# Optimization experiments

Measured on AMD Instinct MI355X. Metric: run time of the kernel, lower is better.

Reference implementation:

```python
import jax, jax.numpy as jnp
import numpy as np

NUM_HEADS = 8
NEG_LARGE = -1e9  # stands in for -inf under the causal mask; masked entries get exactly 0 entmax weight


def _entmax15(z):
    """Exact 1.5-entmax along the last axis (Peters & Martins 2019 sort-based algorithm)."""
    z = z * 0.5
    zs = -jnp.sort(-z, axis=-1)                      # descending sort
    T = z.shape[-1]
    k = jnp.arange(1, T + 1, dtype=z.dtype)
    mean = jnp.cumsum(zs, axis=-1) / k
    mean_sq = jnp.cumsum(zs * zs, axis=-1) / k
    ss = k * (mean_sq - mean * mean)
    delta = (1.0 - ss) / k
    tau = mean - jnp.sqrt(jnp.maximum(delta, 0.0))
    support = jnp.sum(tau <= zs, axis=-1, keepdims=True)      # support size >= 1
    tau_star = jnp.take_along_axis(tau, support - 1, axis=-1)
    return jnp.square(jnp.maximum(z - tau_star, 0.0))


def setup_inputs() -> dict:
    key = jax.random.key(0)
    ks = jax.random.split(key, 9)
    B, T, D, H = 2, 2048, 512, NUM_HEADS
    dk = D // H
    s = 1.0 / np.sqrt(D)
    so = 1.0 / np.sqrt(dk)
    x = jax.random.normal(ks[0], (B, T, D), jnp.float32)
    Wq = jax.random.uniform(ks[1], (D, D), jnp.float32, -s, s)
    bq = jax.random.uniform(ks[2], (D,), jnp.float32, -s, s)
    Wk = jax.random.uniform(ks[3], (D, D), jnp.float32, -s, s)
    bk = jax.random.uniform(ks[4], (D,), jnp.float32, -s, s)
    Wv = jax.random.uniform(ks[5], (D, D), jnp.float32, -s, s)
    bv = jax.random.uniform(ks[6], (D,), jnp.float32, -s, s)
    Wo = jax.random.uniform(ks[7], (dk, D), jnp.float32, -so, so)
    bo = jax.random.uniform(ks[8], (D,), jnp.float32, -so, so)
    return {"x": x, "Wq": Wq, "bq": bq, "Wk": Wk, "bk": bk, "Wv": Wv, "bv": bv, "Wo": Wo, "bo": bo}


def reference(x, Wq, bq, Wk, bk, Wv, bv, Wo, bo):
    B, T, D = x.shape
    H = NUM_HEADS
    dk = D // H
    Q = (x @ Wq + bq).reshape(B, T, H, dk).transpose(0, 2, 1, 3)   # [B,H,T,dk]
    K = (x @ Wk + bk).reshape(B, T, H, dk).transpose(0, 2, 1, 3)
    V = (x @ Wv + bv).reshape(B, T, H, dk).transpose(0, 2, 1, 3)
    scores = jnp.einsum('bhtd,bhsd->bhts', Q, K) / np.float32(np.sqrt(dk))
    causal = jnp.triu(jnp.ones((T, T), bool), k=1)                 # True above diagonal
    scores = jnp.where(causal[None, None, :, :], jnp.float32(NEG_LARGE), scores)
    weights = _entmax15(scores)                                    # [B,H,T,T]
    weights_avg = weights.mean(axis=1)                             # [B,T,T]
    V_combined = V.mean(axis=1)                                    # [B,T,dk]
    out = jnp.einsum('bts,bsd->btd', weights_avg, V_combined)      # [B,T,dk]
    return out @ Wo + bo, weights_avg
```

## Files before the change

kernel.cpp:

```cpp
#include <hip/hip_runtime.h>
#include <hip/hip_bf16.h>
#include <cstdint>

#define B_ 2
#define T_ 2048
#define D_ 512
#define H_ 8
#define DK_ 64
#define TQ_ 4
#define NT_ (T_ / TQ_)
#define M_ (B_ * T_)

__global__ __launch_bounds__(256) void gemm_bias_kernel(
    const float* __restrict__ A, const float* __restrict__ W,
    const float* __restrict__ bias, float* __restrict__ C,
    int M, int N, int K)
{
  __shared__ float As[16][68];
  __shared__ float Bs[16][68];
  const int bm = blockIdx.y * 64;
  const int bn = blockIdx.x * 64;
  const int tid = threadIdx.x;
  const int tx = tid & 15, ty = tid >> 4;
  float acc[4][4] = {};
  for (int k0 = 0; k0 < K; k0 += 16) {
    {
      const int r = tid >> 2;
      const int c = (tid & 3) << 2;
      const float4 a = *reinterpret_cast<const float4*>(&A[(size_t)(bm + r) * K + k0 + c]);
      As[c + 0][r] = a.x; As[c + 1][r] = a.y; As[c + 2][r] = a.z; As[c + 3][r] = a.w;
    }
    {
      const int r = tid >> 4;
      const int c = (tid & 15) << 2;
      *reinterpret_cast<float4*>(&Bs[r][c]) =
          *reinterpret_cast<const float4*>(&W[(size_t)(k0 + r) * N + bn + c]);
    }
    __syncthreads();
#pragma unroll
    for (int kk = 0; kk < 16; ++kk) {
      float av[4], bv[4];
#pragma unroll
      for (int i = 0; i < 4; ++i) av[i] = As[kk][ty * 4 + i];
#pragma unroll
      for (int j = 0; j < 4; ++j) bv[j] = Bs[kk][tx * 4 + j];
#pragma unroll
      for (int i = 0; i < 4; ++i)
#pragma unroll
        for (int j = 0; j < 4; ++j) acc[i][j] += av[i] * bv[j];
    }
    __syncthreads();
  }
#pragma unroll
  for (int i = 0; i < 4; ++i) {
    const int row = bm + ty * 4 + i;
#pragma unroll
    for (int j = 0; j < 4; ++j) {
      const int col = bn + tx * 4 + j;
      C[(size_t)row * N + col] = acc[i][j] + bias[col];
    }
  }
}

__global__ __launch_bounds__(256) void gemm_bias_kernelT(
    const float* __restrict__ A, const float* __restrict__ W,
    const float* __restrict__ bias, float* __restrict__ Ct,
    int M, int N, int K)
{
  __shared__ float As[16][68];
  __shared__ float Bs[16][68];
  const int bm = blockIdx.y * 64;
  const int bn = blockIdx.x * 64;
  const int tid = threadIdx.x;
  const int tx = tid & 15, ty = tid >> 4;
  float acc[4][4] = {};
  for (int k0 = 0; k0 < K; k0 += 16) {
    {
      const int r = tid >> 2;
      const int c = (tid & 3) << 2;
      const float4 a = *reinterpret_cast<const float4*>(&A[(size_t)(bm + r) * K + k0 + c]);
      As[c + 0][r] = a.x; As[c + 1][r] = a.y; As[c + 2][r] = a.z; As[c + 3][r] = a.w;
    }
    {
      const int r = tid >> 4;
      const int c = (tid & 15) << 2;
      *reinterpret_cast<float4*>(&Bs[r][c]) =
          *reinterpret_cast<const float4*>(&W[(size_t)(k0 + r) * N + bn + c]);
    }
    __syncthreads();
#pragma unroll
    for (int kk = 0; kk < 16; ++kk) {
      float av[4], bv[4];
#pragma unroll
      for (int i = 0; i < 4; ++i) av[i] = As[kk][ty * 4 + i];
#pragma unroll
      for (int j = 0; j < 4; ++j) bv[j] = Bs[kk][tx * 4 + j];
#pragma unroll
      for (int i = 0; i < 4; ++i)
#pragma unroll
        for (int j = 0; j < 4; ++j) acc[i][j] += av[i] * bv[j];
    }
    __syncthreads();
  }
#pragma unroll
  for (int j = 0; j < 4; ++j) {
    const int col = bn + tx * 4 + j;
    const float bb = bias[col];
    const float4 v = make_float4(acc[0][j] + bb, acc[1][j] + bb, acc[2][j] + bb, acc[3][j] + bb);
    *reinterpret_cast<float4*>(&Ct[(size_t)col * M + bm + ty * 4]) = v;
  }
}

__global__ __launch_bounds__(256) void vcombine_kernel(const float* __restrict__ V,
                                                       float* __restrict__ Vc)
{
  const int idx = blockIdx.x * 256 + threadIdx.x;
  if (idx >= M_ * DK_) return;
  const int row = idx >> 6, d = idx & 63;
  float s = 0.f;
#pragma unroll
  for (int h = 0; h < H_; ++h) s += V[(size_t)row * D_ + h * DK_ + d];
  Vc[idx] = s * 0.125f;
}

__global__ __launch_bounds__(256, 4)
__attribute__((amdgpu_waves_per_eu(4, 4)))
void attn_kernel(
    const float* __restrict__ Qg, const float* __restrict__ Kt,
    const float* __restrict__ Vc, float* __restrict__ wavg,
    float* __restrict__ attn_out)
{
  __shared__ float sc[TQ_][T_];
  __shared__ float4 qs4[TQ_][16];
  __shared__ float part[4][TQ_][DK_];

  const int tid = threadIdx.x;
  const int b = blockIdx.x & 1;
  const int tile = (NT_ - 1) - (blockIdx.x >> 1);
  const int t0 = tile * TQ_;
  const int nS = t0 + TQ_;
  const int wave = __builtin_amdgcn_readfirstlane(tid >> 6);
  const int lane = tid & 63;
  const int n = t0 + wave + 1;
  float* const scw = &sc[wave][0];

  float wacc[32];
#pragma unroll
  for (int j = 0; j < 32; ++j) wacc[j] = 0.f;

  for (int h = 0; h < H_; ++h) {
    __syncthreads();
    if (tid < TQ_ * 16) {
      const int r = tid >> 4, d4 = tid & 15;
      qs4[r][d4] = *reinterpret_cast<const float4*>(
          &Qg[(size_t)(b * T_ + t0 + r) * D_ + h * DK_ + d4 * 4]);
    }
    __syncthreads();

    for (int s0 = tid * 4; s0 < nS; s0 += 1024) {
      const float* Ktp = &Kt[(size_t)(h * DK_) * M_ + b * T_ + s0];
      float4 acc0 = {}, acc1 = {}, acc2 = {}, acc3 = {};
#pragma unroll 2
      for (int d4 = 0; d4 < 16; ++d4) {
        const float4 q0 = qs4[0][d4];
        const float4 q1 = qs4[1][d4];
        const float4 q2 = qs4[2][d4];
        const float4 q3 = qs4[3][d4];
        const float4 k0 = *reinterpret_cast<const float4*>(Ktp + (size_t)(d4 * 4 + 0) * M_);
        const float4 k1 = *reinterpret_cast<const float4*>(Ktp + (size_t)(d4 * 4 + 1) * M_);
        const float4 k2 = *reinterpret_cast<const float4*>(Ktp + (size_t)(d4 * 4 + 2) * M_);
        const float4 k3 = *reinterpret_cast<const float4*>(Ktp + (size_t)(d4 * 4 + 3) * M_);
#define FMA4(a, qv, kv) a.x = fmaf(qv, kv.x, a.x); a.y = fmaf(qv, kv.y, a.y); \
                        a.z = fmaf(qv, kv.z, a.z); a.w = fmaf(qv, kv.w, a.w)
        FMA4(acc0, q0.x, k0); FMA4(acc0, q0.y, k1); FMA4(acc0, q0.z, k2); FMA4(acc0, q0.w, k3);
        FMA4(acc1, q1.x, k0); FMA4(acc1, q1.y, k1); FMA4(acc1, q1.z, k2); FMA4(acc1, q1.w, k3);
        FMA4(acc2, q2.x, k0); FMA4(acc2, q2.y, k1); FMA4(acc2, q2.z, k2); FMA4(acc2, q2.w, k3);
        FMA4(acc3, q3.x, k0); FMA4(acc3, q3.y, k1); FMA4(acc3, q3.z, k2); FMA4(acc3, q3.w, k3);
#undef FMA4
      }
      acc0.x *= 0.0625f; acc0.y *= 0.0625f; acc0.z *= 0.0625f; acc0.w *= 0.0625f;
      acc1.x *= 0.0625f; acc1.y *= 0.0625f; acc1.z *= 0.0625f; acc1.w *= 0.0625f;
      acc2.x *= 0.0625f; acc2.y *= 0.0625f; acc2.z *= 0.0625f; acc2.w *= 0.0625f;
      acc3.x *= 0.0625f; acc3.y *= 0.0625f; acc3.z *= 0.0625f; acc3.w *= 0.0625f;
      *reinterpret_cast<float4*>(&sc[0][s0]) = acc0;
      *reinterpret_cast<float4*>(&sc[1][s0]) = acc1;
      *reinterpret_cast<float4*>(&sc[2][s0]) = acc2;
      *reinterpret_cast<float4*>(&sc[3][s0]) = acc3;
    }
    __syncthreads();

    float srow[32];
#pragma unroll
    for (int j = 0; j < 32; ++j) {
      if (j * 64 < n) {
        const int s = lane + j * 64;
        const float v = scw[s];
        srow[j] = (s < n) ? v : -1e30f;
      }
    }
    asm volatile("" ::: "memory");

    float mx = -1e30f;
#pragma unroll
    for (int j = 0; j < 32; ++j)
      if (j * 64 < n) mx = fmaxf(mx, srow[j]);
#pragma unroll
    for (int m = 32; m >= 1; m >>= 1) mx = fmaxf(mx, __shfl_xor(mx, m, 64));

    float tau = mx - 1.0f;
#pragma unroll 1
    for (int it = 0; it < 16; ++it) {
      float s1 = 0.f, s2 = 0.f;
#pragma unroll
      for (int j = 0; j < 32; ++j) {
        if (j * 64 < n) {
          const float u = fmaxf(srow[j] - tau, 0.f);
          s1 += u;
          s2 = fmaf(u, u, s2);
        }
      }
#pragma unroll
      for (int m = 32; m >= 1; m >>= 1) {
        s1 += __shfl_xor(s1, m, 64);
        s2 += __shfl_xor(s2, m, 64);
      }
      if (s2 - 1.0f < 1e-5f) break;
      tau += (s2 - 1.0f) / fmaxf(2.f * s1, 1e-12f);
    }
    tau = fminf(tau, mx - 1e-8f);

#pragma unroll
    for (int j = 0; j < 32; ++j) {
      if (j * 64 < n) {
        const float u = fmaxf(srow[j] - tau, 0.f);
        wacc[j] = fmaf(u, u, wacc[j]);
      }
    }
  }
  __syncthreads();

#pragma unroll
  for (int j = 0; j < 32; ++j) scw[lane + j * 64] = wacc[j];
  __syncthreads();

  for (int i4 = tid; i4 < TQ_ * T_ / 4; i4 += 256) {
    const int r = i4 >> 9;
    const int c4 = i4 & 511;
    float4 w = reinterpret_cast<const float4*>(&sc[r][0])[c4];
    w.x *= 0.125f; w.y *= 0.125f; w.z *= 0.125f; w.w *= 0.125f;
    reinterpret_cast<float4*>(&wavg[(size_t)(b * T_ + t0 + r) * T_])[c4] = w;
  }

  {
    const int sg = wave, dd = lane;
    float acc0 = 0.f, acc1 = 0.f, acc2 = 0.f, acc3 = 0.f;
    for (int s = sg; s < nS; s += 4) {
      const float v = Vc[(size_t)(b * T_ + s) * DK_ + dd];
      acc0 += sc[0][s] * v;
      acc1 += sc[1][s] * v;
      acc2 += sc[2][s] * v;
      acc3 += sc[3][s] * v;
    }
    part[sg][0][dd] = acc0;
    part[sg][1][dd] = acc1;
    part[sg][2][dd] = acc2;
    part[sg][3][dd] = acc3;
  }
  __syncthreads();
  {
    const int r = wave, dd = lane;
    const float o = (part[0][r][dd] + part[1][r][dd] + part[2][r][dd] + part[3][r][dd]) * 0.125f;
    attn_out[(size_t)(b * T_ + t0 + r) * DK_ + dd] = o;
  }
}

extern "C" void kernel_launch(void* const* d_in, const int* in_sizes, int n_in,
                              void* d_out, int out_size, void* d_ws, size_t ws_size,
                              hipStream_t stream)
{
  const float* x  = (const float*)d_in[0];
  const float* Wq = (const float*)d_in[1];
  const float* bq = (const float*)d_in[2];
  const float* Wk = (const float*)d_in[3];
  const float* bk = (const float*)d_in[4];
  const float* Wv = (const float*)d_in[5];
  const float* bv = (const float*)d_in[6];
  const float* Wo = (const float*)d_in[7];
  const float* bo = (const float*)d_in[8];
  float* out = (float*)d_out;
  float* ws  = (float*)d_ws;

  float* Q  = ws;
  float* Kt = Q + (size_t)M_ * D_;
  float* V  = Kt + (size_t)D_ * M_;
  float* Vc = V + (size_t)M_ * D_;
  float* AO = Vc + (size_t)M_ * DK_;

  float* out1 = out;
  float* wavg = out + (size_t)M_ * D_;

  const dim3 gp(D_ / 64, M_ / 64);
  gemm_bias_kernel <<<gp, 256, 0, stream>>>(x, Wq, bq, Q,  M_, D_, D_);
  gemm_bias_kernelT<<<gp, 256, 0, stream>>>(x, Wk, bk, Kt, M_, D_, D_);
  gemm_bias_kernel <<<gp, 256, 0, stream>>>(x, Wv, bv, V,  M_, D_, D_);
  vcombine_kernel<<<(M_ * DK_ + 255) / 256, 256, 0, stream>>>(V, Vc);
  attn_kernel<<<B_ * NT_, 256, 0, stream>>>(Q, Kt, Vc, wavg, AO);
  gemm_bias_kernel<<<gp, 256, 0, stream>>>(AO, Wo, bo, out1, M_, D_, DK_);
}
```

Measured before the change: 405.5 us.

## Double query tile to 8 rows, prefetch next-head Q, add exact-support tau steps

Grows the attention block to 8 query rows with 512 threads, so each K column load feeds twice as many rows. The next head's Q slice is double-buffered and loaded during the entmax phase, which removes one barrier per head. The tau solver now starts with three exact support-based closed-form updates before switching to Newton steps, and the iteration cap drops from 16 to 12, aiming for fewer reduction rounds. The trade-offs are higher register pressure from eight float4 accumulators, half as many blocks, and a stop test that now uses the absolute error.

```diff
diff --git a/kernel.cpp b/kernel.cpp
--- a/kernel.cpp
+++ b/kernel.cpp
@@ -7,8 +7,8 @@
 #define D_ 512
 #define H_ 8
 #define DK_ 64
-#define TQ_ 4
-#define NT_ (T_ / TQ_)
+#define TQ_ 8
+#define NTL_ (T_ / TQ_)
 #define M_ (B_ * T_)
 
 __global__ __launch_bounds__(256) void gemm_bias_kernel(
@@ -123,20 +123,19 @@
   Vc[idx] = s * 0.125f;
 }
 
-__global__ __launch_bounds__(256, 4)
-__attribute__((amdgpu_waves_per_eu(4, 4)))
+__global__ __launch_bounds__(512, 4)
 void attn_kernel(
     const float* __restrict__ Qg, const float* __restrict__ Kt,
     const float* __restrict__ Vc, float* __restrict__ wavg,
     float* __restrict__ attn_out)
 {
   __shared__ float sc[TQ_][T_];
-  __shared__ float4 qs4[TQ_][16];
+  __shared__ float4 qs4[2][TQ_][16];
   __shared__ float part[4][TQ_][DK_];
 
   const int tid = threadIdx.x;
   const int b = blockIdx.x & 1;
-  const int tile = (NT_ - 1) - (blockIdx.x >> 1);
+  const int tile = (NTL_ - 1) - (blockIdx.x >> 1);
   const int t0 = tile * TQ_;
   const int nS = t0 + TQ_;
   const int wave = __builtin_amdgcn_readfirstlane(tid >> 6);
@@ -148,46 +147,52 @@
 #pragma unroll
   for (int j = 0; j < 32; ++j) wacc[j] = 0.f;
 
+  if (tid < TQ_ * 16) {
+    const int r = tid >> 4, d4 = tid & 15;
+    qs4[0][r][d4] = *reinterpret_cast<const float4*>(
+        &Qg[(size_t)(b * T_ + t0 + r) * D_ + 0 * DK_ + d4 * 4]);
+  }
+  __syncthreads();
+
   for (int h = 0; h < H_; ++h) {
-    __syncthreads();
-    if (tid < TQ_ * 16) {
-      const int r = tid >> 4, d4 = tid & 15;
-      qs4[r][d4] = *reinterpret_cast<const float4*>(
-          &Qg[(size_t)(b * T_ + t0 + r) * D_ + h * DK_ + d4 * 4]);
-    }
-    __syncthreads();
-
-    for (int s0 = tid * 4; s0 < nS; s0 += 1024) {
+    const int s0 = tid * 4;
+    if (s0 < nS) {
       const float* Ktp = &Kt[(size_t)(h * DK_) * M_ + b * T_ + s0];
-      float4 acc0 = {}, acc1 = {}, acc2 = {}, acc3 = {};
+      float4 a[TQ_];
+#pragma unroll
+      for (int r = 0; r < TQ_; ++r) a[r] = make_float4(0.f, 0.f, 0.f, 0.f);
 #pragma unroll 2
       for (int d4 = 0; d4 < 16; ++d4) {
-        const float4 q0 = qs4[0][d4];
-        const float4 q1 = qs4[1][d4];
-        const float4 q2 = qs4[2][d4];
-        const float4 q3 = qs4[3][d4];
         const float4 k0 = *reinterpret_cast<const float4*>(Ktp + (size_t)(d4 * 4 + 0) * M_);
         const float4 k1 = *reinterpret_cast<const float4*>(Ktp + (size_t)(d4 * 4 + 1) * M_);
         const float4 k2 = *reinterpret_cast<const float4*>(Ktp + (size_t)(d4 * 4 + 2) * M_);
         const float4 k3 = *reinterpret_cast<const float4*>(Ktp + (size_t)(d4 * 4 + 3) * M_);
-#define FMA4(a, qv, kv) a.x = fmaf(qv, kv.x, a.x); a.y = fmaf(qv, kv.y, a.y); \
-                        a.z = fmaf(qv, kv.z, a.z); a.w = fmaf(qv, kv.w, a.w)
-        FMA4(acc0, q0.x, k0); FMA4(acc0, q0.y, k1); FMA4(acc0, q0.z, k2); FMA4(acc0, q0.w, k3);
-        FMA4(acc1, q1.x, k0); FMA4(acc1, q1.y, k1); FMA4(acc1, q1.z, k2); FMA4(acc1, q1.w, k3);
-        FMA4(acc2, q2.x, k0); FMA4(acc2, q2.y, k1); FMA4(acc2, q2.z, k2); FMA4(acc2, q2.w, k3);
-        FMA4(acc3, q3.x, k0); FMA4(acc3, q3.y, k1); FMA4(acc3, q3.z, k2); FMA4(acc3, q3.w, k3);
-#undef FMA4
-      }
-      acc0.x *= 0.0625f; acc0.y *= 0.0625f; acc0.z *= 0.0625f; acc0.w *= 0.0625f;
-      acc1.x *= 0.0625f; acc1.y *= 0.0625f; acc1.z *= 0.0625f; acc1.w *= 0.0625f;
-      acc2.x *= 0.0625f; acc2.y *= 0.0625f; acc2.z *= 0.0625f; acc2.w *= 0.0625f;
-      acc3.x *= 0.0625f; acc3.y *= 0.0625f; acc3.z *= 0.0625f; acc3.w *= 0.0625f;
-      *reinterpret_cast<float4*>(&sc[0][s0]) = acc0;
-      *reinterpret_cast<float4*>(&sc[1][s0]) = acc1;
-      *reinterpret_cast<float4*>(&sc[2][s0]) = acc2;
-      *reinterpret_cast<float4*>(&sc[3][s0]) = acc3;
-    }
-    __syncthreads();
+#pragma unroll
+        for (int r = 0; r < TQ_; ++r) {
+          const float4 q = qs4[h & 1][r][d4];
+          a[r].x = fmaf(q.x, k0.x, a[r].x); a[r].y = fmaf(q.x, k0.y, a[r].y);
+          a[r].z = fmaf(q.x, k0.z, a[r].z); a[r].w = fmaf(q.x, k0.w, a[r].w);
+          a[r].x = fmaf(q.y, k1.x, a[r].x); a[r].y = fmaf(q.y, k1.y, a[r].y);
+          a[r].z = fmaf(q.y, k1.z, a[r].z); a[r].w = fmaf(q.y, k1.w, a[r].w);
+          a[r].x = fmaf(q.z, k2.x, a[r].x); a[r].y = fmaf(q.z, k2.y, a[r].y);
+          a[r].z = fmaf(q.z, k2.z, a[r].z); a[r].w = fmaf(q.z, k2.w, a[r].w);
+          a[r].x = fmaf(q.w, k3.x, a[r].x); a[r].y = fmaf(q.w, k3.y, a[r].y);
+          a[r].z = fmaf(q.w, k3.z, a[r].z); a[r].w = fmaf(q.w, k3.w, a[r].w);
+        }
+      }
+#pragma unroll
+      for (int r = 0; r < TQ_; ++r) {
+        a[r].x *= 0.0625f; a[r].y *= 0.0625f; a[r].z *= 0.0625f; a[r].w *= 0.0625f;
+        *reinterpret_cast<float4*>(&sc[r][s0]) = a[r];
+      }
+    }
+    __syncthreads();
+
+    if (h + 1 < H_ && tid < TQ_ * 16) {
+      const int r = tid >> 4, d4 = tid & 15;
+      qs4[(h + 1) & 1][r][d4] = *reinterpret_cast<const float4*>(
+          &Qg[(size_t)(b * T_ + t0 + r) * D_ + (h + 1) * DK_ + d4 * 4]);
+    }
 
     float srow[32];
 #pragma unroll
@@ -198,7 +203,6 @@
         srow[j] = (s < n) ? v : -1e30f;
       }
     }
-    asm volatile("" ::: "memory");
 
     float mx = -1e30f;
 #pragma unroll
@@ -209,14 +213,15 @@
 
     float tau = mx - 1.0f;
 #pragma unroll 1
-    for (int it = 0; it < 16; ++it) {
-      float s1 = 0.f, s2 = 0.f;
+    for (int it = 0; it < 12; ++it) {
+      float s1 = 0.f, s2 = 0.f, cn = 0.f;
 #pragma unroll
       for (int j = 0; j < 32; ++j) {
         if (j * 64 < n) {
           const float u = fmaxf(srow[j] - tau, 0.f);
           s1 += u;
           s2 = fmaf(u, u, s2);
+          cn += (u > 0.f) ? 1.f : 0.f;
         }
       }
 #pragma unroll
@@ -224,8 +229,17 @@
         s1 += __shfl_xor(s1, m, 64);
         s2 += __shfl_xor(s2, m, 64);
       }
-      if (s2 - 1.0f < 1e-5f) break;
-      tau += (s2 - 1.0f) / fmaxf(2.f * s1, 1e-12f);
+      if (fabsf(s2 - 1.0f) < 1e-5f) break;
+      if (it < 3) {
+#pragma unroll
+        for (int m = 32; m >= 1; m >>= 1) cn += __shfl_xor(cn, m, 64);
+        const float kf = fmaxf(cn, 1.f);
+        const float mu = tau + s1 / kf;
+        const float ss = s2 - s1 * s1 / kf;
+        tau = mu - sqrtf(fmaxf((1.0f - ss) / kf, 0.f));
+      } else {
+        tau += (s2 - 1.0f) / fmaxf(2.f * s1, 1e-12f);
+      }
     }
     tau = fminf(tau, mx - 1e-8f);
 
@@ -236,14 +250,14 @@
         wacc[j] = fmaf(u, u, wacc[j]);
       }
     }
-  }
-  __syncthreads();
+    __syncthreads();
+  }
 
 #pragma unroll
   for (int j = 0; j < 32; ++j) scw[lane + j * 64] = wacc[j];
   __syncthreads();
 
-  for (int i4 = tid; i4 < TQ_ * T_ / 4; i4 += 256) {
+  for (int i4 = tid; i4 < TQ_ * T_ / 4; i4 += 512) {
     const int r = i4 >> 9;
     const int c4 = i4 & 511;
     float4 w = reinterpret_cast<const float4*>(&sc[r][0])[c4];
@@ -252,25 +266,27 @@
   }
 
   {
-    const int sg = wave, dd = lane;
-    float acc0 = 0.f, acc1 = 0.f, acc2 = 0.f, acc3 = 0.f;
+    const int sg = wave & 3;
+    const int rb = (wave >> 2) * 4;
+    float a0 = 0.f, a1 = 0.f, a2 = 0.f, a3 = 0.f;
     for (int s = sg; s < nS; s += 4) {
-      const float v = Vc[(size_t)(b * T_ + s) * DK_ + dd];
-      acc0 += sc[0][s] * v;
-      acc1 += sc[1][s] * v;
-      acc2 += sc[2][s] * v;
-      acc3 += sc[3][s] * v;
-    }
-    part[sg][0][dd] = acc0;
-    part[sg][1][dd] = acc1;
-    part[sg][2][dd] = acc2;
-    part[sg][3][dd] = acc3;
+      const float v = Vc[(size_t)(b * T_ + s) * DK_ + lane];
+      a0 += sc[rb + 0][s] * v;
+      a1 += sc[rb + 1][s] * v;
+      a2 += sc[rb + 2][s] * v;
+      a3 += sc[rb + 3][s] * v;
+    }
+    part[sg][rb + 0][lane] = a0;
+    part[sg][rb + 1][lane] = a1;
+    part[sg][rb + 2][lane] = a2;
+    part[sg][rb + 3][lane] = a3;
   }
   __syncthreads();
   {
-    const int r = wave, dd = lane;
-    const float o = (part[0][r][dd] + part[1][r][dd] + part[2][r][dd] + part[3][r][dd]) * 0.125f;
-    attn_out[(size_t)(b * T_ + t0 + r) * DK_ + dd] = o;
+    const int r = wave;
+    const float o = (part[0][r][lane] + part[1][r][lane] +
+                     part[2][r][lane] + part[3][r][lane]) * 0.125f;
+    attn_out[(size_t)(b * T_ + t0 + r) * DK_ + lane] = o;
   }
 }
 
@@ -304,6 +320,6 @@
   gemm_bias_kernelT<<<gp, 256, 0, stream>>>(x, Wk, bk, Kt, M_, D_, D_);
   gemm_bias_kernel <<<gp, 256, 0, stream>>>(x, Wv, bv, V,  M_, D_, D_);
   vcombine_kernel<<<(M_ * DK_ + 255) / 256, 256, 0, stream>>>(V, Vc);
-  attn_kernel<<<B_ * NT_, 256, 0, stream>>>(Q, Kt, Vc, wavg, AO);
+  attn_kernel<<<B_ * NTL_, 512, 0, stream>>>(Q, Kt, Vc, wavg, AO);
   gemm_bias_kernel<<<gp, 256, 0, stream>>>(AO, Wo, bo, out1, M_, D_, DK_);
 }
```

Result: no change. 402.4 us (-0.8%).
